# Kernel optimization log

Hardware: AMD Instinct MI355X
Metric: run time of the kernel (lower is better)

## Reference

```python
import jax, jax.numpy as jnp
import numpy as np

EMB = 1024
HEADS = 8
SEQ = 4096
LN_EPS = 1e-5


def _layernorm(x, g, b):
    mu = jnp.mean(x, axis=-1, keepdims=True)
    var = jnp.mean(jnp.square(x - mu), axis=-1, keepdims=True)
    return (x - mu) * jax.lax.rsqrt(var + LN_EPS) * g + b


def setup_inputs() -> dict:
    key = jax.random.key(0)
    ks = jax.random.split(key, 12)
    s = 1.0 / np.sqrt(EMB)
    sz = 1.0 / np.sqrt(EMB * HEADS)
    return {
        "history": jax.random.normal(ks[0], (SEQ, EMB), jnp.float32),
        "embdding": jax.random.normal(ks[1], (SEQ, EMB), jnp.float32),
        # per-head Linear weights, torch layout [out, in], stacked over heads
        "Wq_w": jax.random.uniform(ks[2], (HEADS, EMB, EMB), jnp.float32, -s, s),
        "Wq_b": jax.random.uniform(ks[3], (HEADS, EMB), jnp.float32, -s, s),
        "Wk_w": jax.random.uniform(ks[4], (HEADS, EMB, EMB), jnp.float32, -s, s),
        "Wk_b": jax.random.uniform(ks[5], (HEADS, EMB), jnp.float32, -s, s),
        "Wv_w": jax.random.uniform(ks[6], (HEADS, EMB, EMB), jnp.float32, -s, s),
        "Wv_b": jax.random.uniform(ks[7], (HEADS, EMB), jnp.float32, -s, s),
        "Wz_w": jax.random.uniform(ks[8], (EMB, EMB * HEADS), jnp.float32, -sz, sz),
        "Wz_b": jax.random.uniform(ks[9], (EMB,), jnp.float32, -sz, sz),
        "ln1_g": jnp.ones((EMB,), jnp.float32),
        "ln1_b": jnp.zeros((EMB,), jnp.float32),
        "Wf_w": jax.random.uniform(ks[10], (EMB, EMB), jnp.float32, -s, s),
        "Wf_b": jax.random.uniform(ks[11], (EMB,), jnp.float32, -s, s),
        "ln2_g": jnp.ones((EMB,), jnp.float32),
        "ln2_b": jnp.zeros((EMB,), jnp.float32),
    }


def reference(history, embdding, Wq_w, Wq_b, Wk_w, Wk_b, Wv_w, Wv_b,
              Wz_w, Wz_b, ln1_g, ln1_b, Wf_w, Wf_b, ln2_g, ln2_b):
    S, E = embdding.shape
    H = Wq_w.shape[0]
    # per-head linears (torch: y = x @ W.T + b), batched over heads
    Q = jnp.einsum('se,hfe->hsf', embdding, Wq_w) + Wq_b[:, None, :]  # [H,S,E]
    K = jnp.einsum('se,hfe->hsf', embdding, Wk_w) + Wk_b[:, None, :]
    V = jnp.einsum('se,hfe->hsf', history, Wv_w) + Wv_b[:, None, :]
    # K^T @ Q -> [H, E, E], softmax over dim=1 of the 2D matrix == last axis here
    scores = jnp.einsum('hse,hsf->hef', K, Q) / jnp.sqrt(jnp.asarray(E, Q.dtype))
    A = jax.nn.softmax(scores, axis=-1)  # [H,E,E]
    Zh = jnp.einsum('hse,hef->hsf', V, A)  # [H,S,E]
    Z = jnp.transpose(Zh, (1, 0, 2)).reshape(S, H * E)  # cat(dim=1) in head order
    O = Z @ Wz_w.T + Wz_b  # [S,E]
    LN1 = _layernorm(O, ln1_g, ln1_b) + embdding
    FN = LN1 @ Wf_w.T + Wf_b
    LN2 = _layernorm(FN, ln2_g, ln2_b) + LN1
    return LN2
```

## Files before the change

### kernel.cpp

```cpp
#include <hip/hip_runtime.h>


constexpr int EMB = 1024;
constexpr int SEQ = 4096;
constexpr int NH  = 8;

using f32x4  = __attribute__((ext_vector_type(4))) float;
using bf16x8 = __attribute__((ext_vector_type(8))) __bf16;
using us8    = __attribute__((ext_vector_type(8))) unsigned short;

#define GLOAD_LDS16(g, l) __builtin_amdgcn_global_load_lds(                 \
    (const __attribute__((address_space(1))) void*)(g),                     \
    (__attribute__((address_space(3))) void*)(l), 16, 0, 0)

__device__ inline unsigned short f2bf(float x) {
  unsigned int u = __float_as_uint(x);
  u += 0x7FFFu + ((u >> 16) & 1u);
  return (unsigned short)(u >> 16);
}
__device__ inline float bf2f(unsigned short h) {
  return __uint_as_float(((unsigned int)h) << 16);
}

constexpr int NB_DOTB = 4096;
constexpr int NB_ROWB = 1664;
constexpr int NB_XT   = 1024;

__global__ __launch_bounds__(256) void mega_cvt_k(
    const float* __restrict__ Wk, const float* __restrict__ Wq,
    const float* __restrict__ hist, const float* __restrict__ Wz,
    const float* __restrict__ Wf, const float* __restrict__ emb,
    const float* __restrict__ Wv, const float* __restrict__ xbar,
    unsigned short* __restrict__ Wkb, unsigned short* __restrict__ Wqb,
    unsigned short* __restrict__ Yb, unsigned short* __restrict__ Wzb,
    unsigned short* __restrict__ Wfb, unsigned short* __restrict__ XT,
    unsigned short* __restrict__ WvT,
    float* __restrict__ u, float* __restrict__ v) {
  __shared__ float tileT[64][65];
  const int b = blockIdx.x, tid = threadIdx.x;

  if (b < NB_DOTB) {
    int gw = b * 4 + (tid >> 6);
    int lane = tid & 63;
    const float* src = (gw < 8192) ? Wk : Wq;
    unsigned short* dst = (gw < 8192) ? Wkb : Wqb;
    float* dot = (gw < 8192) ? u : v;
    int row = gw & 8191;
    const float4* sr = (const float4*)(src + (size_t)row * EMB);
    const float4* xb4 = (const float4*)xbar;
    ushort4* d4 = (ushort4*)(dst + (size_t)row * EMB);
    float s = 0.f;
#pragma unroll
    for (int j = 0; j < 4; ++j) {
      int idx = j * 64 + lane;
      float4 x = sr[idx];
      float4 xb = xb4[idx];
      ushort4 o; o.x = f2bf(x.x); o.y = f2bf(x.y); o.z = f2bf(x.z); o.w = f2bf(x.w);
      d4[idx] = o;
      s += x.x * xb.x + x.y * xb.y + x.z * xb.z + x.w * xb.w;
    }
#pragma unroll
    for (int off = 32; off; off >>= 1) s += __shfl_down(s, off);
    if (lane == 0) dot[row] = s;
  } else if (b < NB_DOTB + NB_ROWB) {
    size_t f0 = (size_t)(b - NB_DOTB) * 8192;
    const float* src; unsigned short* dst; size_t loc;
    if (f0 < 4194304ull) { src = hist; dst = Yb; loc = f0; }
    else if (f0 < 12582912ull) { src = Wz; dst = Wzb; loc = f0 - 4194304ull; }
    else { src = Wf; dst = Wfb; loc = f0 - 12582912ull; }
#pragma unroll
    for (int p = 0; p < 8; ++p) {
      int i = p * 256 + tid;
      float4 x = ((const float4*)(src + loc))[i];
      ushort4 o; o.x = f2bf(x.x); o.y = f2bf(x.y); o.z = f2bf(x.z); o.w = f2bf(x.w);
      ((ushort4*)(dst + loc))[i] = o;
    }
  } else {
    int tb = b - (NB_DOTB + NB_ROWB);
    const float* src; unsigned short* dst; int R, r0, c0;
    if (tb < NB_XT) {
      src = emb; dst = XT; R = SEQ;
      r0 = (tb >> 4) * 64; c0 = (tb & 15) * 64;
    } else {
      int t2 = tb - NB_XT, z = t2 >> 8, tt = t2 & 255;
      src = Wv + (size_t)z * EMB * EMB; dst = WvT + (size_t)z * EMB * EMB;
      R = EMB;
      r0 = (tt >> 4) * 64; c0 = (tt & 15) * 64;
    }
    int tx = tid & 15, ty = tid >> 4;
#pragma unroll
    for (int p = 0; p < 4; ++p) {
      int ir = p * 16 + ty;
      float4 x = *(const float4*)(src + (size_t)(r0 + ir) * EMB + c0 + tx * 4);
      tileT[tx * 4 + 0][ir] = x.x; tileT[tx * 4 + 1][ir] = x.y;
      tileT[tx * 4 + 2][ir] = x.z; tileT[tx * 4 + 3][ir] = x.w;
    }
    __syncthreads();
#pragma unroll
    for (int p = 0; p < 4; ++p) {
      int orow = p * 16 + ty;
      ushort4 o;
      o.x = f2bf(tileT[orow][tx * 4 + 0]);
      o.y = f2bf(tileT[orow][tx * 4 + 1]);
      o.z = f2bf(tileT[orow][tx * 4 + 2]);
      o.w = f2bf(tileT[orow][tx * 4 + 3]);
      *(ushort4*)(dst + (size_t)(c0 + orow) * R + r0 + tx * 4) = o;
    }
  }
}

__global__ __launch_bounds__(256) void colsum_part_k(const float* __restrict__ X,
                                                     float* __restrict__ part) {
  int e = blockIdx.x * 256 + threadIdx.x;
  int y = blockIdx.y;
  float s = 0.f;
  for (int r = y * 128; r < y * 128 + 128; ++r) s += X[(size_t)r * EMB + e];
  part[y * EMB + e] = s;
}
__global__ __launch_bounds__(256) void colsum_red_k(const float* __restrict__ part,
                                                    float* __restrict__ xbar) {
  int e = blockIdx.x * 256 + threadIdx.x;
  float s = 0.f;
  for (int y = 0; y < 32; ++y) s += part[y * EMB + e];
  xbar[e] = s;
}

__global__ __launch_bounds__(256) void dvec_k(const unsigned short* __restrict__ Wzb,
                                              const float* __restrict__ bz,
                                              const float* __restrict__ c,
                                              float* __restrict__ d) {
  __shared__ float sb[4];
  int g = blockIdx.x, tid = threadIdx.x;
  const unsigned short* row = Wzb + (size_t)g * (NH * EMB);
  float s = 0.f;
#pragma unroll
  for (int p = 0; p < 4; ++p) {
    int i = p * 256 + tid;
    us8 w = ((const us8*)row)[i];
    float4 c0 = ((const float4*)c)[i * 2];
    float4 c1 = ((const float4*)c)[i * 2 + 1];
    s += bf2f(w[0]) * c0.x + bf2f(w[1]) * c0.y + bf2f(w[2]) * c0.z + bf2f(w[3]) * c0.w;
    s += bf2f(w[4]) * c1.x + bf2f(w[5]) * c1.y + bf2f(w[6]) * c1.z + bf2f(w[7]) * c1.w;
  }
  int lane = tid & 63, w = tid >> 6;
#pragma unroll
  for (int off = 32; off; off >>= 1) s += __shfl_down(s, off);
  if (lane == 0) sb[w] = s;
  __syncthreads();
  if (tid == 0) d[g] = bz[g] + sb[0] + sb[1] + sb[2] + sb[3];
}

__global__ __launch_bounds__(256) void mred_tr_k(const unsigned short* __restrict__ Mp,
                                                 unsigned short* __restrict__ MT) {
  __shared__ float t[32][33];
  int g0 = blockIdx.x * 32, e0 = blockIdx.y * 32;
  int tx = threadIdx.x & 31, ty = threadIdx.x >> 5;
#pragma unroll
  for (int k = 0; k < 4; ++k) {
    int e = e0 + ty + k * 8;
    float s = 0.f;
#pragma unroll
    for (int h = 0; h < NH; ++h)
      s += bf2f(Mp[((size_t)h << 20) + (size_t)e * EMB + g0 + tx]);
    t[ty + k * 8][tx] = s;
  }
  __syncthreads();
#pragma unroll
  for (int k = 0; k < 4; ++k) {
    int r = ty + k * 8;
    MT[(size_t)(g0 + r) * EMB + e0 + tx] = f2bf(t[tx][r]);
  }
}

__global__ __launch_bounds__(256) void gram_red_k(const unsigned short* __restrict__ Gp,
                                                  unsigned short* __restrict__ Gbf) {
  int i = blockIdx.x * 256 + threadIdx.x;
  float4 s = {0.f, 0.f, 0.f, 0.f};
#pragma unroll
  for (int z = 0; z < 8; ++z) {
    ushort4 v = ((const ushort4*)(Gp + (size_t)z * EMB * EMB))[i];
    s.x += bf2f(v.x); s.y += bf2f(v.y); s.z += bf2f(v.z); s.w += bf2f(v.w);
  }
  ushort4 o; o.x = f2bf(s.x); o.y = f2bf(s.y); o.z = f2bf(s.z); o.w = f2bf(s.w);
  ((ushort4*)Gbf)[i] = o;
}

__global__ __launch_bounds__(256) void colstat1_k(const unsigned short* __restrict__ ScT,
                                                  float* __restrict__ m_part,
                                                  float* __restrict__ s_part) {
  int col = blockIdx.x * 256 + threadIdx.x;
  int rc = blockIdx.y, h = blockIdx.z;
  const unsigned short* base = ScT + ((size_t)h * EMB + rc * 64) * EMB + col;
  float m = -1e30f, s = 0.f;
#pragma unroll 4
  for (int r = 0; r < 64; ++r) {
    float x = bf2f(base[(size_t)r * EMB]);
    float nm = fmaxf(m, x);
    s = s * __expf(m - nm) + __expf(x - nm);
    m = nm;
  }
  m_part[((size_t)h * 16 + rc) * EMB + col] = m;
  s_part[((size_t)h * 16 + rc) * EMB + col] = s;
}

__global__ __launch_bounds__(256) void colstat2_k(const float* __restrict__ m_part,
                                                  const float* __restrict__ s_part,
                                                  float* __restrict__ mfin,
                                                  float* __restrict__ isfin) {
  int i = blockIdx.x * 256 + threadIdx.x;
  int h = i >> 10, col = i & 1023;
  float M = -1e30f, S = 0.f;
#pragma unroll
  for (int c = 0; c < 16; ++c) {
    float m = m_part[((size_t)h * 16 + c) * EMB + col];
    float s = s_part[((size_t)h * 16 + c) * EMB + col];
    float nm = fmaxf(M, m);
    S = S * __expf(M - nm) + s * __expf(m - nm);
    M = nm;
  }
  mfin[i] = M;
  isfin[i] = 1.0f / S;
}

__global__ __launch_bounds__(256) void at_cvec_k(const unsigned short* __restrict__ ScT,
                                                 const float* __restrict__ mfin,
                                                 const float* __restrict__ isfin,
                                                 const float* __restrict__ bv,
                                                 unsigned short* __restrict__ AT,
                                                 float* __restrict__ cbuf) {
  __shared__ float sb[4];
  int f = blockIdx.x, h = blockIdx.y, tid = threadIdx.x;
  size_t rowoff = ((size_t)h * EMB + f) * EMB;
  ushort4 xr = ((const ushort4*)(ScT + rowoff))[tid];
  float4 m  = ((const float4*)(mfin + (size_t)h * EMB))[tid];
  float4 is = ((const float4*)(isfin + (size_t)h * EMB))[tid];
  float4 b  = ((const float4*)(bv + (size_t)h * EMB))[tid];
  float a0 = __expf(bf2f(xr.x) - m.x) * is.x;
  float a1 = __expf(bf2f(xr.y) - m.y) * is.y;
  float a2 = __expf(bf2f(xr.z) - m.z) * is.z;
  float a3 = __expf(bf2f(xr.w) - m.w) * is.w;
  ushort4 o; o.x = f2bf(a0); o.y = f2bf(a1); o.z = f2bf(a2); o.w = f2bf(a3);
  ((ushort4*)(AT + rowoff))[tid] = o;
  float s = a0 * b.x + a1 * b.y + a2 * b.z + a3 * b.w;
  int lane = tid & 63, w = tid >> 6;
#pragma unroll
  for (int off = 32; off; off >>= 1) s += __shfl_down(s, off);
  if (lane == 0) sb[w] = s;
  __syncthreads();
  if (tid == 0) cbuf[h * EMB + f] = sb[0] + sb[1] + sb[2] + sb[3];
}

__global__ __launch_bounds__(256) void layernorm_k(const float* __restrict__ Xin,
                                                   const float* __restrict__ resid,
                                                   const float* __restrict__ gw,
                                                   const float* __restrict__ bw,
                                                   float* __restrict__ outf,
                                                   unsigned short* __restrict__ outb) {
  __shared__ float sb[16];
  int row = blockIdx.x, tid = threadIdx.x;
  float4 v = ((const float4*)(Xin + (size_t)row * EMB))[tid];
  float s = v.x + v.y + v.z + v.w;
  float q = v.x * v.x + v.y * v.y + v.z * v.z + v.w * v.w;
  int lane = tid & 63, w = tid >> 6;
#pragma unroll
  for (int off = 32; off; off >>= 1) { s += __shfl_down(s, off); q += __shfl_down(q, off); }
  if (lane == 0) { sb[w] = s; sb[8 + w] = q; }
  __syncthreads();
  float mu  = (sb[0] + sb[1] + sb[2] + sb[3]) * (1.0f / EMB);
  float var = (sb[8] + sb[9] + sb[10] + sb[11]) * (1.0f / EMB) - mu * mu;
  float rs = rsqrtf(var + 1e-5f);
  float4 rv = ((const float4*)(resid + (size_t)row * EMB))[tid];
  float4 gv = ((const float4*)gw)[tid];
  float4 bv = ((const float4*)bw)[tid];
  float o0 = (v.x - mu) * rs * gv.x + bv.x + rv.x;
  float o1 = (v.y - mu) * rs * gv.y + bv.y + rv.y;
  float o2 = (v.z - mu) * rs * gv.z + bv.z + rv.z;
  float o3 = (v.w - mu) * rs * gv.w + bv.w + rv.w;
  float4 ov; ov.x = o0; ov.y = o1; ov.z = o2; ov.w = o3;
  ((float4*)(outf + (size_t)row * EMB))[tid] = ov;
  if (outb) {
    ushort4 ob; ob.x = f2bf(o0); ob.y = f2bf(o1); ob.z = f2bf(o2); ob.w = f2bf(o3);
    ((ushort4*)(outb + (size_t)row * EMB))[tid] = ob;
  }
}

template <int MODE>
__global__ __launch_bounds__(256) void gemm_nt(const unsigned short* __restrict__ A,
                                               const unsigned short* __restrict__ B,
                                               void* __restrict__ Cout,
                                               int K, int lda, int ldb, int ldc,
                                               long long aZ, long long bZ, long long cZ,
                                               int nx, int ny,
                                               const float* __restrict__ e0,
                                               const float* __restrict__ e1,
                                               const float* __restrict__ e2,
                                               const float* __restrict__ e3) {
  const int q = gridDim.x >> 3;
  const int wg = (blockIdx.x & 7) * q + (blockIdx.x >> 3);
  const int bx = wg % nx;
  const int by = (wg / nx) % ny;
  const int z  = wg / (nx * ny);
  A += (size_t)z * aZ;
  B += (size_t)z * bZ;
  const int tid = threadIdx.x;
  const int lane = tid & 63, wid = tid >> 6;
  const int wm = wid >> 1, wn = wid & 1;
  const int row0 = bx * 128, col0 = by * 128;

  __shared__ __align__(16) unsigned short As[2][128 * 64];
  __shared__ __align__(16) unsigned short Bs[2][128 * 64];

  f32x4 acc[4][4] = {};
  const int lrow = lane & 15, kg = lane >> 4;
  const int lr = lane >> 3;
  const int lc = (lane & 7) * 8;

  auto stage = [&](int buf, int k0) {
#pragma unroll
    for (int c = 0; c < 4; ++c) {
      int chunk = wid * 4 + c;
      int r = chunk * 8 + lr;
      GLOAD_LDS16(A + (size_t)(row0 + r) * lda + k0 + lc, &As[buf][chunk * 512]);
      GLOAD_LDS16(B + (size_t)(col0 + r) * ldb + k0 + lc, &Bs[buf][chunk * 512]);
    }
  };

  stage(0, 0);
  __syncthreads();

  const int nt = K >> 6;
  for (int t = 0; t < nt; ++t) {
    const int cur = t & 1;
    if (t + 1 < nt) stage(cur ^ 1, (t + 1) << 6);
#pragma unroll
    for (int ks = 0; ks < 2; ++ks) {
      bf16x8 a[4], b[4];
      int koff = ks * 32 + kg * 8;
#pragma unroll
      for (int i = 0; i < 4; ++i)
        a[i] = *(const bf16x8*)&As[cur][(wm * 64 + i * 16 + lrow) * 64 + koff];
#pragma unroll
      for (int j = 0; j < 4; ++j)
        b[j] = *(const bf16x8*)&Bs[cur][(wn * 64 + j * 16 + lrow) * 64 + koff];
#pragma unroll
      for (int i = 0; i < 4; ++i)
#pragma unroll
        for (int j = 0; j < 4; ++j)
          acc[i][j] = __builtin_amdgcn_mfma_f32_16x16x32_bf16(a[i], b[j], acc[i][j], 0, 0, 0);
    }
    __syncthreads();
  }

  const int rb = (lane >> 4) * 4, cc = lane & 15;
  if (MODE == 1 || MODE == 4) {
    unsigned short* Cs = &As[0][0];
#pragma unroll
    for (int i = 0; i < 4; ++i) {
#pragma unroll
      for (int j = 0; j < 4; ++j) {
#pragma unroll
        for (int r = 0; r < 4; ++r) {
          float val = acc[i][j][r];
          int mm = wm * 64 + i * 16 + rb + r;
          int nn = wn * 64 + j * 16 + cc;
          if (MODE == 4) {
            int m = row0 + mm, n = col0 + nn;
            float bq = e0[z * EMB + m], uu = e1[z * EMB + n];
            float bk = e2[z * EMB + n], vv = e3[z * EMB + m];
            val = (val + bq * (uu + (float)SEQ * bk) + vv * bk) * (1.0f / 32.0f);
          }
          Cs[mm * 128 + nn] = f2bf(val);
        }
      }
    }
    __syncthreads();
    unsigned short* Cg = (unsigned short*)Cout + (size_t)z * cZ;
#pragma unroll
    for (int p = 0; p < 8; ++p) {
      int idx = p * 256 + tid;
      int row = idx >> 4, col = (idx & 15) * 8;
      *(us8*)(Cg + (size_t)(row0 + row) * ldc + col0 + col) =
          *(const us8*)&Cs[row * 128 + col];
    }
  } else {
#pragma unroll
    for (int i = 0; i < 4; ++i) {
#pragma unroll
      for (int j = 0; j < 4; ++j) {
#pragma unroll
        for (int r = 0; r < 4; ++r) {
          int m = row0 + wm * 64 + i * 16 + rb + r;
          int n = col0 + wn * 64 + j * 16 + cc;
          size_t off = (size_t)z * cZ + (size_t)m * ldc + n;
          ((float*)Cout)[off] = acc[i][j][r] + e0[n];
        }
      }
    }
  }
}

extern "C" void kernel_launch(void* const* d_in, const int* in_sizes, int n_in,
                              void* d_out, int out_size, void* d_ws, size_t ws_size,
                              hipStream_t stream) {
  const float* history = (const float*)d_in[0];
  const float* emb     = (const float*)d_in[1];
  const float* Wq_w = (const float*)d_in[2];
  const float* Wq_b = (const float*)d_in[3];
  const float* Wk_w = (const float*)d_in[4];
  const float* Wk_b = (const float*)d_in[5];
  const float* Wv_w = (const float*)d_in[6];
  const float* Wv_b = (const float*)d_in[7];
  const float* Wz_w = (const float*)d_in[8];
  const float* Wz_b = (const float*)d_in[9];
  const float* ln1_g = (const float*)d_in[10];
  const float* ln1_b = (const float*)d_in[11];
  const float* Wf_w = (const float*)d_in[12];
  const float* Wf_b = (const float*)d_in[13];
  const float* ln2_g = (const float*)d_in[14];
  const float* ln2_b = (const float*)d_in[15];

  char* ws = (char*)d_ws;
  const size_t MB = 1024ull * 1024ull;
  unsigned short* XT  = (unsigned short*)(ws + 0);
  unsigned short* Ybf = (unsigned short*)(ws + 8 * MB);
  unsigned short* Wkb = (unsigned short*)(ws + 16 * MB);
  unsigned short* Wqb = (unsigned short*)(ws + 32 * MB);
  unsigned short* WvT = (unsigned short*)(ws + 48 * MB);
  unsigned short* Wzb = (unsigned short*)(ws + 64 * MB);
  unsigned short* Wfb = (unsigned short*)(ws + 80 * MB);
  unsigned short* Gbf = (unsigned short*)(ws + 82 * MB);
  float* xpart = (float*)(ws + 84 * MB);
  float* xbar  = (float*)(ws + 84 * MB + 160 * 1024);
  float* ubuf  = (float*)(ws + 84 * MB + 192 * 1024);
  float* vbuf  = (float*)(ws + 84 * MB + 256 * 1024);
  float* cbuf  = (float*)(ws + 84 * MB + 320 * 1024);
  float* dbuf  = (float*)(ws + 84 * MB + 384 * 1024);
  unsigned short* Tbf = (unsigned short*)(ws + 85 * MB);
  float* Sc  = (float*)(ws + 101 * MB);
  char*  St  = ws + 133 * MB;
  unsigned short* ATb = (unsigned short*)(ws + 149 * MB);
  unsigned short* MTb = (unsigned short*)(ws + 165 * MB);
  float* m_part = (float*)(St);
  float* s_part = (float*)(St + 512 * 1024);
  float* mfin   = (float*)(St + 1024 * 1024);
  float* isfin  = (float*)(St + 1056 * 1024);
  unsigned short* Gp  = (unsigned short*)Sc;
  unsigned short* ScT = (unsigned short*)Sc;
  unsigned short* Cbf = Tbf;
  unsigned short* Mp  = (unsigned short*)Sc;
  float* Obuf = (float*)St;
  float* LN1  = (float*)ATb;
  unsigned short* LN1b = XT;
  float* FN   = (float*)Tbf;

  colsum_part_k<<<dim3(4, 32), 256, 0, stream>>>(emb, xpart);
  colsum_red_k<<<dim3(4), 256, 0, stream>>>(xpart, xbar);

  mega_cvt_k<<<dim3(8832), 256, 0, stream>>>(Wk_w, Wq_w, history, Wz_w, Wf_w,
                                             emb, Wv_w, xbar,
                                             Wkb, Wqb, Ybf, Wzb, Wfb, XT, WvT,
                                             ubuf, vbuf);

  gemm_nt<1><<<dim3(512), 256, 0, stream>>>(XT, XT, Gp, 512, SEQ, SEQ, EMB,
                                            512, 512, (long long)EMB * EMB, 8, 8,
                                            nullptr, nullptr, nullptr, nullptr);
  gram_red_k<<<dim3(EMB * EMB / 4 / 256), 256, 0, stream>>>(Gp, Gbf);
  gemm_nt<1><<<dim3(512), 256, 0, stream>>>(Wqb, Gbf, Tbf, EMB, EMB, EMB, EMB,
                                            (long long)EMB * EMB, 0, (long long)EMB * EMB, 8, 8,
                                            nullptr, nullptr, nullptr, nullptr);
  gemm_nt<4><<<dim3(512), 256, 0, stream>>>(Tbf, Wkb, ScT, EMB, EMB, EMB, EMB,
                                            (long long)EMB * EMB, (long long)EMB * EMB,
                                            (long long)EMB * EMB, 8, 8,
                                            Wq_b, ubuf, Wk_b, vbuf);
  colstat1_k<<<dim3(4, 16, NH), 256, 0, stream>>>(ScT, m_part, s_part);
  colstat2_k<<<dim3(32), 256, 0, stream>>>(m_part, s_part, mfin, isfin);
  at_cvec_k<<<dim3(EMB, NH), 256, 0, stream>>>(ScT, mfin, isfin, Wv_b, ATb, cbuf);
  gemm_nt<1><<<dim3(512), 256, 0, stream>>>(WvT, ATb, Cbf, EMB, EMB, EMB, EMB,
                                            (long long)EMB * EMB, (long long)EMB * EMB,
                                            (long long)EMB * EMB, 8, 8,
                                            nullptr, nullptr, nullptr, nullptr);
  gemm_nt<1><<<dim3(512), 256, 0, stream>>>(Cbf, Wzb, Mp, EMB, EMB, NH * EMB, EMB,
                                            (long long)EMB * EMB, (long long)EMB,
                                            (long long)EMB * EMB, 8, 8,
                                            nullptr, nullptr, nullptr, nullptr);
  mred_tr_k<<<dim3(EMB / 32, EMB / 32), 256, 0, stream>>>(Mp, MTb);
  dvec_k<<<dim3(EMB), 256, 0, stream>>>(Wzb, Wz_b, cbuf, dbuf);
  gemm_nt<3><<<dim3(256), 256, 0, stream>>>(Ybf, MTb, Obuf, EMB, EMB, EMB, EMB,
                                            0, 0, 0, 32, 8,
                                            dbuf, nullptr, nullptr, nullptr);
  layernorm_k<<<dim3(SEQ), 256, 0, stream>>>(Obuf, emb, ln1_g, ln1_b, LN1, LN1b);
  gemm_nt<3><<<dim3(256), 256, 0, stream>>>(LN1b, Wfb, FN, EMB, EMB, EMB, EMB,
                                            0, 0, 0, 32, 8,
                                            Wf_b, nullptr, nullptr, nullptr);
  layernorm_k<<<dim3(SEQ), 256, 0, stream>>>(FN, LN1, ln2_g, ln2_b, (float*)d_out, nullptr);
}
```

Baseline: 298.2 us.

## Fuse fp32-to-bf16 conversion of weights and history into GEMM tile loads

Drops the standalone conversion pass that wrote bf16 copies of Wk, Wq, Wz, Wf and history. The GEMMs now take fp32 operands directly and convert them to bf16 while loading each tile into LDS, using register loads in place of the async global-to-LDS path. The row dot products and the dvec reduction now read the fp32 weights directly. This removes a large bf16 write and re-read, but costs in-kernel conversion, synchronous loads that lose the direct-to-LDS copy, and repeated reading of fp32 data (twice the bytes) across tiles.

```diff
diff --git a/kernel.cpp b/kernel.cpp
--- a/kernel.cpp
+++ b/kernel.cpp
@@ -22,91 +22,66 @@
   return __uint_as_float(((unsigned int)h) << 16);
 }
 
-constexpr int NB_DOTB = 4096;
-constexpr int NB_ROWB = 1664;
-constexpr int NB_XT   = 1024;
-
-__global__ __launch_bounds__(256) void mega_cvt_k(
-    const float* __restrict__ Wk, const float* __restrict__ Wq,
-    const float* __restrict__ hist, const float* __restrict__ Wz,
-    const float* __restrict__ Wf, const float* __restrict__ emb,
-    const float* __restrict__ Wv, const float* __restrict__ xbar,
-    unsigned short* __restrict__ Wkb, unsigned short* __restrict__ Wqb,
-    unsigned short* __restrict__ Yb, unsigned short* __restrict__ Wzb,
-    unsigned short* __restrict__ Wfb, unsigned short* __restrict__ XT,
-    unsigned short* __restrict__ WvT,
-    float* __restrict__ u, float* __restrict__ v) {
+__global__ __launch_bounds__(256) void cvt_tr_k(const float* __restrict__ emb,
+                                                const float* __restrict__ Wv,
+                                                unsigned short* __restrict__ XT,
+                                                unsigned short* __restrict__ WvT) {
   __shared__ float tileT[64][65];
   const int b = blockIdx.x, tid = threadIdx.x;
-
-  if (b < NB_DOTB) {
-    int gw = b * 4 + (tid >> 6);
-    int lane = tid & 63;
-    const float* src = (gw < 8192) ? Wk : Wq;
-    unsigned short* dst = (gw < 8192) ? Wkb : Wqb;
-    float* dot = (gw < 8192) ? u : v;
-    int row = gw & 8191;
-    const float4* sr = (const float4*)(src + (size_t)row * EMB);
-    const float4* xb4 = (const float4*)xbar;
-    ushort4* d4 = (ushort4*)(dst + (size_t)row * EMB);
-    float s = 0.f;
-#pragma unroll
-    for (int j = 0; j < 4; ++j) {
-      int idx = j * 64 + lane;
-      float4 x = sr[idx];
-      float4 xb = xb4[idx];
-      ushort4 o; o.x = f2bf(x.x); o.y = f2bf(x.y); o.z = f2bf(x.z); o.w = f2bf(x.w);
-      d4[idx] = o;
-      s += x.x * xb.x + x.y * xb.y + x.z * xb.z + x.w * xb.w;
-    }
-#pragma unroll
-    for (int off = 32; off; off >>= 1) s += __shfl_down(s, off);
-    if (lane == 0) dot[row] = s;
-  } else if (b < NB_DOTB + NB_ROWB) {
-    size_t f0 = (size_t)(b - NB_DOTB) * 8192;
-    const float* src; unsigned short* dst; size_t loc;
-    if (f0 < 4194304ull) { src = hist; dst = Yb; loc = f0; }
-    else if (f0 < 12582912ull) { src = Wz; dst = Wzb; loc = f0 - 4194304ull; }
-    else { src = Wf; dst = Wfb; loc = f0 - 12582912ull; }
-#pragma unroll
-    for (int p = 0; p < 8; ++p) {
-      int i = p * 256 + tid;
-      float4 x = ((const float4*)(src + loc))[i];
-      ushort4 o; o.x = f2bf(x.x); o.y = f2bf(x.y); o.z = f2bf(x.z); o.w = f2bf(x.w);
-      ((ushort4*)(dst + loc))[i] = o;
-    }
+  const float* src; unsigned short* dst; int R, r0, c0;
+  if (b < 1024) {
+    src = emb; dst = XT; R = SEQ;
+    r0 = (b >> 4) * 64; c0 = (b & 15) * 64;
   } else {
-    int tb = b - (NB_DOTB + NB_ROWB);
-    const float* src; unsigned short* dst; int R, r0, c0;
-    if (tb < NB_XT) {
-      src = emb; dst = XT; R = SEQ;
-      r0 = (tb >> 4) * 64; c0 = (tb & 15) * 64;
-    } else {
-      int t2 = tb - NB_XT, z = t2 >> 8, tt = t2 & 255;
-      src = Wv + (size_t)z * EMB * EMB; dst = WvT + (size_t)z * EMB * EMB;
-      R = EMB;
-      r0 = (tt >> 4) * 64; c0 = (tt & 15) * 64;
-    }
-    int tx = tid & 15, ty = tid >> 4;
-#pragma unroll
-    for (int p = 0; p < 4; ++p) {
-      int ir = p * 16 + ty;
-      float4 x = *(const float4*)(src + (size_t)(r0 + ir) * EMB + c0 + tx * 4);
-      tileT[tx * 4 + 0][ir] = x.x; tileT[tx * 4 + 1][ir] = x.y;
-      tileT[tx * 4 + 2][ir] = x.z; tileT[tx * 4 + 3][ir] = x.w;
-    }
-    __syncthreads();
-#pragma unroll
-    for (int p = 0; p < 4; ++p) {
-      int orow = p * 16 + ty;
-      ushort4 o;
-      o.x = f2bf(tileT[orow][tx * 4 + 0]);
-      o.y = f2bf(tileT[orow][tx * 4 + 1]);
-      o.z = f2bf(tileT[orow][tx * 4 + 2]);
-      o.w = f2bf(tileT[orow][tx * 4 + 3]);
-      *(ushort4*)(dst + (size_t)(c0 + orow) * R + r0 + tx * 4) = o;
-    }
-  }
+    int t2 = b - 1024, z = t2 >> 8, tt = t2 & 255;
+    src = Wv + (size_t)z * EMB * EMB; dst = WvT + (size_t)z * EMB * EMB;
+    R = EMB;
+    r0 = (tt >> 4) * 64; c0 = (tt & 15) * 64;
+  }
+  int tx = tid & 15, ty = tid >> 4;
+#pragma unroll
+  for (int p = 0; p < 4; ++p) {
+    int ir = p * 16 + ty;
+    float4 x = *(const float4*)(src + (size_t)(r0 + ir) * EMB + c0 + tx * 4);
+    tileT[tx * 4 + 0][ir] = x.x; tileT[tx * 4 + 1][ir] = x.y;
+    tileT[tx * 4 + 2][ir] = x.z; tileT[tx * 4 + 3][ir] = x.w;
+  }
+  __syncthreads();
+#pragma unroll
+  for (int p = 0; p < 4; ++p) {
+    int orow = p * 16 + ty;
+    ushort4 o;
+    o.x = f2bf(tileT[orow][tx * 4 + 0]);
+    o.y = f2bf(tileT[orow][tx * 4 + 1]);
+    o.z = f2bf(tileT[orow][tx * 4 + 2]);
+    o.w = f2bf(tileT[orow][tx * 4 + 3]);
+    *(ushort4*)(dst + (size_t)(c0 + orow) * R + r0 + tx * 4) = o;
+  }
+}
+
+__global__ __launch_bounds__(256) void uv_k(const float* __restrict__ Wk,
+                                            const float* __restrict__ Wq,
+                                            const float* __restrict__ xbar,
+                                            float* __restrict__ u,
+                                            float* __restrict__ v) {
+  int gw = blockIdx.x * 4 + (threadIdx.x >> 6);
+  int lane = threadIdx.x & 63;
+  const float* src = (gw < 8192) ? Wk : Wq;
+  float* dot = (gw < 8192) ? u : v;
+  int row = gw & 8191;
+  const float4* sr  = (const float4*)(src + (size_t)row * EMB);
+  const float4* xb4 = (const float4*)xbar;
+  float s = 0.f;
+#pragma unroll
+  for (int j = 0; j < 4; ++j) {
+    int idx = j * 64 + lane;
+    float4 x = sr[idx];
+    float4 xb = xb4[idx];
+    s += x.x * xb.x + x.y * xb.y + x.z * xb.z + x.w * xb.w;
+  }
+#pragma unroll
+  for (int off = 32; off; off >>= 1) s += __shfl_down(s, off);
+  if (lane == 0) dot[row] = s;
 }
 
 __global__ __launch_bounds__(256) void colsum_part_k(const float* __restrict__ X,
@@ -125,22 +100,20 @@
   xbar[e] = s;
 }
 
-__global__ __launch_bounds__(256) void dvec_k(const unsigned short* __restrict__ Wzb,
+__global__ __launch_bounds__(256) void dvec_k(const float* __restrict__ Wz,
                                               const float* __restrict__ bz,
                                               const float* __restrict__ c,
                                               float* __restrict__ d) {
   __shared__ float sb[4];
   int g = blockIdx.x, tid = threadIdx.x;
-  const unsigned short* row = Wzb + (size_t)g * (NH * EMB);
+  const float* row = Wz + (size_t)g * (NH * EMB);
   float s = 0.f;
 #pragma unroll
-  for (int p = 0; p < 4; ++p) {
+  for (int p = 0; p < 8; ++p) {
     int i = p * 256 + tid;
-    us8 w = ((const us8*)row)[i];
-    float4 c0 = ((const float4*)c)[i * 2];
-    float4 c1 = ((const float4*)c)[i * 2 + 1];
-    s += bf2f(w[0]) * c0.x + bf2f(w[1]) * c0.y + bf2f(w[2]) * c0.z + bf2f(w[3]) * c0.w;
-    s += bf2f(w[4]) * c1.x + bf2f(w[5]) * c1.y + bf2f(w[6]) * c1.z + bf2f(w[7]) * c1.w;
+    float4 w = ((const float4*)row)[i];
+    float4 cv = ((const float4*)c)[i];
+    s += w.x * cv.x + w.y * cv.y + w.z * cv.z + w.w * cv.w;
   }
   int lane = tid & 63, w = tid >> 6;
 #pragma unroll
@@ -284,9 +257,9 @@
   }
 }
 
-template <int MODE>
-__global__ __launch_bounds__(256) void gemm_nt(const unsigned short* __restrict__ A,
-                                               const unsigned short* __restrict__ B,
+template <int MODE, int AF32, int BF32>
+__global__ __launch_bounds__(256) void gemm_nt(const void* __restrict__ Av,
+                                               const void* __restrict__ Bv,
                                                void* __restrict__ Cout,
                                                int K, int lda, int ldb, int ldc,
                                                long long aZ, long long bZ, long long cZ,
@@ -300,8 +273,10 @@
   const int bx = wg % nx;
   const int by = (wg / nx) % ny;
   const int z  = wg / (nx * ny);
-  A += (size_t)z * aZ;
-  B += (size_t)z * bZ;
+  const unsigned short* A16 = AF32 ? nullptr : (const unsigned short*)Av + (size_t)z * aZ;
+  const unsigned short* B16 = BF32 ? nullptr : (const unsigned short*)Bv + (size_t)z * bZ;
+  const float* A32 = AF32 ? (const float*)Av + (size_t)z * aZ : nullptr;
+  const float* B32 = BF32 ? (const float*)Bv + (size_t)z * bZ : nullptr;
   const int tid = threadIdx.x;
   const int lane = tid & 63, wid = tid >> 6;
   const int wm = wid >> 1, wn = wid & 1;
@@ -320,8 +295,28 @@
     for (int c = 0; c < 4; ++c) {
       int chunk = wid * 4 + c;
       int r = chunk * 8 + lr;
-      GLOAD_LDS16(A + (size_t)(row0 + r) * lda + k0 + lc, &As[buf][chunk * 512]);
-      GLOAD_LDS16(B + (size_t)(col0 + r) * ldb + k0 + lc, &Bs[buf][chunk * 512]);
+      if (AF32) {
+        const float* src = A32 + (size_t)(row0 + r) * lda + k0 + lc;
+        float4 x0 = *(const float4*)src;
+        float4 x1 = *(const float4*)(src + 4);
+        us8 o;
+        o[0] = f2bf(x0.x); o[1] = f2bf(x0.y); o[2] = f2bf(x0.z); o[3] = f2bf(x0.w);
+        o[4] = f2bf(x1.x); o[5] = f2bf(x1.y); o[6] = f2bf(x1.z); o[7] = f2bf(x1.w);
+        *(us8*)&As[buf][chunk * 512 + lane * 8] = o;
+      } else {
+        GLOAD_LDS16(A16 + (size_t)(row0 + r) * lda + k0 + lc, &As[buf][chunk * 512]);
+      }
+      if (BF32) {
+        const float* src = B32 + (size_t)(col0 + r) * ldb + k0 + lc;
+        float4 x0 = *(const float4*)src;
+        float4 x1 = *(const float4*)(src + 4);
+        us8 o;
+        o[0] = f2bf(x0.x); o[1] = f2bf(x0.y); o[2] = f2bf(x0.z); o[3] = f2bf(x0.w);
+        o[4] = f2bf(x1.x); o[5] = f2bf(x1.y); o[6] = f2bf(x1.z); o[7] = f2bf(x1.w);
+        *(us8*)&Bs[buf][chunk * 512 + lane * 8] = o;
+      } else {
+        GLOAD_LDS16(B16 + (size_t)(col0 + r) * ldb + k0 + lc, &Bs[buf][chunk * 512]);
+      }
     }
   };
 
@@ -422,12 +417,7 @@
   char* ws = (char*)d_ws;
   const size_t MB = 1024ull * 1024ull;
   unsigned short* XT  = (unsigned short*)(ws + 0);
-  unsigned short* Ybf = (unsigned short*)(ws + 8 * MB);
-  unsigned short* Wkb = (unsigned short*)(ws + 16 * MB);
-  unsigned short* Wqb = (unsigned short*)(ws + 32 * MB);
   unsigned short* WvT = (unsigned short*)(ws + 48 * MB);
-  unsigned short* Wzb = (unsigned short*)(ws + 64 * MB);
-  unsigned short* Wfb = (unsigned short*)(ws + 80 * MB);
   unsigned short* Gbf = (unsigned short*)(ws + 82 * MB);
   float* xpart = (float*)(ws + 84 * MB);
   float* xbar  = (float*)(ws + 84 * MB + 160 * 1024);
@@ -452,45 +442,41 @@
   float* LN1  = (float*)ATb;
   unsigned short* LN1b = XT;
   float* FN   = (float*)Tbf;
+  const long long EE = (long long)EMB * EMB;
 
   colsum_part_k<<<dim3(4, 32), 256, 0, stream>>>(emb, xpart);
   colsum_red_k<<<dim3(4), 256, 0, stream>>>(xpart, xbar);
-
-  mega_cvt_k<<<dim3(8832), 256, 0, stream>>>(Wk_w, Wq_w, history, Wz_w, Wf_w,
-                                             emb, Wv_w, xbar,
-                                             Wkb, Wqb, Ybf, Wzb, Wfb, XT, WvT,
-                                             ubuf, vbuf);
-
-  gemm_nt<1><<<dim3(512), 256, 0, stream>>>(XT, XT, Gp, 512, SEQ, SEQ, EMB,
-                                            512, 512, (long long)EMB * EMB, 8, 8,
-                                            nullptr, nullptr, nullptr, nullptr);
+  uv_k<<<dim3(4096), 256, 0, stream>>>(Wk_w, Wq_w, xbar, ubuf, vbuf);
+
+  cvt_tr_k<<<dim3(3072), 256, 0, stream>>>(emb, Wv_w, XT, WvT);
+
+  gemm_nt<1, 0, 0><<<dim3(512), 256, 0, stream>>>(XT, XT, Gp, 512, SEQ, SEQ, EMB,
+                                                  512, 512, EE, 8, 8,
+                                                  nullptr, nullptr, nullptr, nullptr);
   gram_red_k<<<dim3(EMB * EMB / 4 / 256), 256, 0, stream>>>(Gp, Gbf);
-  gemm_nt<1><<<dim3(512), 256, 0, stream>>>(Wqb, Gbf, Tbf, EMB, EMB, EMB, EMB,
-                                            (long long)EMB * EMB, 0, (long long)EMB * EMB, 8, 8,
-                                            nullptr, nullptr, nullptr, nullptr);
-  gemm_nt<4><<<dim3(512), 256, 0, stream>>>(Tbf, Wkb, ScT, EMB, EMB, EMB, EMB,
-                                            (long long)EMB * EMB, (long long)EMB * EMB,
-                                            (long long)EMB * EMB, 8, 8,
-                                            Wq_b, ubuf, Wk_b, vbuf);
+  gemm_nt<1, 1, 0><<<dim3(512), 256, 0, stream>>>(Wq_w, Gbf, Tbf, EMB, EMB, EMB, EMB,
+                                                  EE, 0, EE, 8, 8,
+                                                  nullptr, nullptr, nullptr, nullptr);
+  gemm_nt<4, 0, 1><<<dim3(512), 256, 0, stream>>>(Tbf, Wk_w, ScT, EMB, EMB, EMB, EMB,
+                                                  EE, EE, EE, 8, 8,
+                                                  Wq_b, ubuf, Wk_b, vbuf);
   colstat1_k<<<dim3(4, 16, NH), 256, 0, stream>>>(ScT, m_part, s_part);
   colstat2_k<<<dim3(32), 256, 0, stream>>>(m_part, s_part, mfin, isfin);
   at_cvec_k<<<dim3(EMB, NH), 256, 0, stream>>>(ScT, mfin, isfin, Wv_b, ATb, cbuf);
-  gemm_nt<1><<<dim3(512), 256, 0, stream>>>(WvT, ATb, Cbf, EMB, EMB, EMB, EMB,
-                                            (long long)EMB * EMB, (long long)EMB * EMB,
-                                            (long long)EMB * EMB, 8, 8,
-                                            nullptr, nullptr, nullptr, nullptr);
-  gemm_nt<1><<<dim3(512), 256, 0, stream>>>(Cbf, Wzb, Mp, EMB, EMB, NH * EMB, EMB,
-                                            (long long)EMB * EMB, (long long)EMB,
-                                            (long long)EMB * EMB, 8, 8,
-                                            nullptr, nullptr, nullptr, nullptr);
+  gemm_nt<1, 0, 0><<<dim3(512), 256, 0, stream>>>(WvT, ATb, Cbf, EMB, EMB, EMB, EMB,
+                                                  EE, EE, EE, 8, 8,
+                                                  nullptr, nullptr, nullptr, nullptr);
+  gemm_nt<1, 0, 1><<<dim3(512), 256, 0, stream>>>(Cbf, Wz_w, Mp, EMB, EMB, NH * EMB, EMB,
+                                                  EE, (long long)EMB, EE, 8, 8,
+                                                  nullptr, nullptr, nullptr, nullptr);
   mred_tr_k<<<dim3(EMB / 32, EMB / 32), 256, 0, stream>>>(Mp, MTb);
-  dvec_k<<<dim3(EMB), 256, 0, stream>>>(Wzb, Wz_b, cbuf, dbuf);
-  gemm_nt<3><<<dim3(256), 256, 0, stream>>>(Ybf, MTb, Obuf, EMB, EMB, EMB, EMB,
-                                            0, 0, 0, 32, 8,
-                                            dbuf, nullptr, nullptr, nullptr);
+  dvec_k<<<dim3(EMB), 256, 0, stream>>>(Wz_w, Wz_b, cbuf, dbuf);
+  gemm_nt<3, 1, 0><<<dim3(256), 256, 0, stream>>>(history, MTb, Obuf, EMB, EMB, EMB, EMB,
+                                                  0, 0, 0, 32, 8,
+                                                  dbuf, nullptr, nullptr, nullptr);
   layernorm_k<<<dim3(SEQ), 256, 0, stream>>>(Obuf, emb, ln1_g, ln1_b, LN1, LN1b);
-  gemm_nt<3><<<dim3(256), 256, 0, stream>>>(LN1b, Wfb, FN, EMB, EMB, EMB, EMB,
-                                            0, 0, 0, 32, 8,
-                                            Wf_b, nullptr, nullptr, nullptr);
+  gemm_nt<3, 0, 1><<<dim3(256), 256, 0, stream>>>(LN1b, Wf_w, FN, EMB, EMB, EMB, EMB,
+                                                  0, 0, 0, 32, 8,
+                                                  Wf_b, nullptr, nullptr, nullptr);
   layernorm_k<<<dim3(SEQ), 256, 0, stream>>>(FN, LN1, ln2_g, ln2_b, (float*)d_out, nullptr);
 }
```

New measurement: 318.7 us. 6.9% more time.

## Halve GEMM M-tile to 64 and drop LDS double buffering for occupancy

Applied to the files above, without the earlier changes.

The shared NT GEMM kernel moves from a 128x128 tile to a 64x128 tile. Each wave now holds 2x4 accumulators, and the double-buffered LDS staging becomes a single buffer with a sync after each load, cutting LDS from 64KB to 24KB per block. All launches double their grid sizes to match, so there are more workgroups to fill the CUs and higher occupancy. In exchange, global loads no longer overlap compute within a block, operand reuse per tile drops, and there are more blocks to schedule.

```diff
diff --git a/kernel.cpp b/kernel.cpp
--- a/kernel.cpp
+++ b/kernel.cpp
@@ -305,45 +305,45 @@
   const int tid = threadIdx.x;
   const int lane = tid & 63, wid = tid >> 6;
   const int wm = wid >> 1, wn = wid & 1;
-  const int row0 = bx * 128, col0 = by * 128;
-
-  __shared__ __align__(16) unsigned short As[2][128 * 64];
-  __shared__ __align__(16) unsigned short Bs[2][128 * 64];
-
-  f32x4 acc[4][4] = {};
+  const int row0 = bx * 64, col0 = by * 128;
+
+  __shared__ __align__(16) unsigned short lds[(64 + 128) * 64];
+  unsigned short* As = lds;
+  unsigned short* Bs = lds + 64 * 64;
+
+  f32x4 acc[2][4] = {};
   const int lrow = lane & 15, kg = lane >> 4;
   const int lr = lane >> 3;
   const int lc = (lane & 7) * 8;
 
-  auto stage = [&](int buf, int k0) {
+  const int nt = K >> 6;
+  for (int t = 0; t < nt; ++t) {
+    const int k0 = t << 6;
+#pragma unroll
+    for (int c = 0; c < 2; ++c) {
+      int chunk = wid * 2 + c;
+      int r = chunk * 8 + lr;
+      GLOAD_LDS16(A + (size_t)(row0 + r) * lda + k0 + lc, &As[chunk * 512]);
+    }
 #pragma unroll
     for (int c = 0; c < 4; ++c) {
       int chunk = wid * 4 + c;
       int r = chunk * 8 + lr;
-      GLOAD_LDS16(A + (size_t)(row0 + r) * lda + k0 + lc, &As[buf][chunk * 512]);
-      GLOAD_LDS16(B + (size_t)(col0 + r) * ldb + k0 + lc, &Bs[buf][chunk * 512]);
-    }
-  };
-
-  stage(0, 0);
-  __syncthreads();
-
-  const int nt = K >> 6;
-  for (int t = 0; t < nt; ++t) {
-    const int cur = t & 1;
-    if (t + 1 < nt) stage(cur ^ 1, (t + 1) << 6);
+      GLOAD_LDS16(B + (size_t)(col0 + r) * ldb + k0 + lc, &Bs[chunk * 512]);
+    }
+    __syncthreads();
 #pragma unroll
     for (int ks = 0; ks < 2; ++ks) {
-      bf16x8 a[4], b[4];
+      bf16x8 a[2], b[4];
       int koff = ks * 32 + kg * 8;
 #pragma unroll
-      for (int i = 0; i < 4; ++i)
-        a[i] = *(const bf16x8*)&As[cur][(wm * 64 + i * 16 + lrow) * 64 + koff];
+      for (int i = 0; i < 2; ++i)
+        a[i] = *(const bf16x8*)&As[(wm * 32 + i * 16 + lrow) * 64 + koff];
 #pragma unroll
       for (int j = 0; j < 4; ++j)
-        b[j] = *(const bf16x8*)&Bs[cur][(wn * 64 + j * 16 + lrow) * 64 + koff];
-#pragma unroll
-      for (int i = 0; i < 4; ++i)
+        b[j] = *(const bf16x8*)&Bs[(wn * 64 + j * 16 + lrow) * 64 + koff];
+#pragma unroll
+      for (int i = 0; i < 2; ++i)
 #pragma unroll
         for (int j = 0; j < 4; ++j)
           acc[i][j] = __builtin_amdgcn_mfma_f32_16x16x32_bf16(a[i], b[j], acc[i][j], 0, 0, 0);
@@ -353,15 +353,15 @@
 
   const int rb = (lane >> 4) * 4, cc = lane & 15;
   if (MODE == 1 || MODE == 4) {
-    unsigned short* Cs = &As[0][0];
-#pragma unroll
-    for (int i = 0; i < 4; ++i) {
+    unsigned short* Cs = lds;
+#pragma unroll
+    for (int i = 0; i < 2; ++i) {
 #pragma unroll
       for (int j = 0; j < 4; ++j) {
 #pragma unroll
         for (int r = 0; r < 4; ++r) {
           float val = acc[i][j][r];
-          int mm = wm * 64 + i * 16 + rb + r;
+          int mm = wm * 32 + i * 16 + rb + r;
           int nn = wn * 64 + j * 16 + cc;
           if (MODE == 4) {
             int m = row0 + mm, n = col0 + nn;
@@ -376,7 +376,7 @@
     __syncthreads();
     unsigned short* Cg = (unsigned short*)Cout + (size_t)z * cZ;
 #pragma unroll
-    for (int p = 0; p < 8; ++p) {
+    for (int p = 0; p < 4; ++p) {
       int idx = p * 256 + tid;
       int row = idx >> 4, col = (idx & 15) * 8;
       *(us8*)(Cg + (size_t)(row0 + row) * ldc + col0 + col) =
@@ -384,12 +384,12 @@
     }
   } else {
 #pragma unroll
-    for (int i = 0; i < 4; ++i) {
+    for (int i = 0; i < 2; ++i) {
 #pragma unroll
       for (int j = 0; j < 4; ++j) {
 #pragma unroll
         for (int r = 0; r < 4; ++r) {
-          int m = row0 + wm * 64 + i * 16 + rb + r;
+          int m = row0 + wm * 32 + i * 16 + rb + r;
           int n = col0 + wn * 64 + j * 16 + cc;
           size_t off = (size_t)z * cZ + (size_t)m * ldc + n;
           ((float*)Cout)[off] = acc[i][j][r] + e0[n];
@@ -452,6 +452,7 @@
   float* LN1  = (float*)ATb;
   unsigned short* LN1b = XT;
   float* FN   = (float*)Tbf;
+  const long long EE = (long long)EMB * EMB;
 
   colsum_part_k<<<dim3(4, 32), 256, 0, stream>>>(emb, xpart);
   colsum_red_k<<<dim3(4), 256, 0, stream>>>(xpart, xbar);
@@ -461,36 +462,33 @@
                                              Wkb, Wqb, Ybf, Wzb, Wfb, XT, WvT,
                                              ubuf, vbuf);
 
-  gemm_nt<1><<<dim3(512), 256, 0, stream>>>(XT, XT, Gp, 512, SEQ, SEQ, EMB,
-                                            512, 512, (long long)EMB * EMB, 8, 8,
-                                            nullptr, nullptr, nullptr, nullptr);
+  gemm_nt<1><<<dim3(1024), 256, 0, stream>>>(XT, XT, Gp, 512, SEQ, SEQ, EMB,
+                                             512, 512, EE, 16, 8,
+                                             nullptr, nullptr, nullptr, nullptr);
   gram_red_k<<<dim3(EMB * EMB / 4 / 256), 256, 0, stream>>>(Gp, Gbf);
-  gemm_nt<1><<<dim3(512), 256, 0, stream>>>(Wqb, Gbf, Tbf, EMB, EMB, EMB, EMB,
-                                            (long long)EMB * EMB, 0, (long long)EMB * EMB, 8, 8,
-                                            nullptr, nullptr, nullptr, nullptr);
-  gemm_nt<4><<<dim3(512), 256, 0, stream>>>(Tbf, Wkb, ScT, EMB, EMB, EMB, EMB,
-                                            (long long)EMB * EMB, (long long)EMB * EMB,
-                                            (long long)EMB * EMB, 8, 8,
-                                            Wq_b, ubuf, Wk_b, vbuf);
+  gemm_nt<1><<<dim3(1024), 256, 0, stream>>>(Wqb, Gbf, Tbf, EMB, EMB, EMB, EMB,
+                                             EE, 0, EE, 16, 8,
+                                             nullptr, nullptr, nullptr, nullptr);
+  gemm_nt<4><<<dim3(1024), 256, 0, stream>>>(Tbf, Wkb, ScT, EMB, EMB, EMB, EMB,
+                                             EE, EE, EE, 16, 8,
+                                             Wq_b, ubuf, Wk_b, vbuf);
   colstat1_k<<<dim3(4, 16, NH), 256, 0, stream>>>(ScT, m_part, s_part);
   colstat2_k<<<dim3(32), 256, 0, stream>>>(m_part, s_part, mfin, isfin);
   at_cvec_k<<<dim3(EMB, NH), 256, 0, stream>>>(ScT, mfin, isfin, Wv_b, ATb, cbuf);
-  gemm_nt<1><<<dim3(512), 256, 0, stream>>>(WvT, ATb, Cbf, EMB, EMB, EMB, EMB,
-                                            (long long)EMB * EMB, (long long)EMB * EMB,
-                                            (long long)EMB * EMB, 8, 8,
-                                            nullptr, nullptr, nullptr, nullptr);
-  gemm_nt<1><<<dim3(512), 256, 0, stream>>>(Cbf, Wzb, Mp, EMB, EMB, NH * EMB, EMB,
-                                            (long long)EMB * EMB, (long long)EMB,
-                                            (long long)EMB * EMB, 8, 8,
-                                            nullptr, nullptr, nullptr, nullptr);
+  gemm_nt<1><<<dim3(1024), 256, 0, stream>>>(WvT, ATb, Cbf, EMB, EMB, EMB, EMB,
+                                             EE, EE, EE, 16, 8,
+                                             nullptr, nullptr, nullptr, nullptr);
+  gemm_nt<1><<<dim3(1024), 256, 0, stream>>>(Cbf, Wzb, Mp, EMB, EMB, NH * EMB, EMB,
+                                             EE, (long long)EMB, EE, 16, 8,
+                                             nullptr, nullptr, nullptr, nullptr);
   mred_tr_k<<<dim3(EMB / 32, EMB / 32), 256, 0, stream>>>(Mp, MTb);
   dvec_k<<<dim3(EMB), 256, 0, stream>>>(Wzb, Wz_b, cbuf, dbuf);
-  gemm_nt<3><<<dim3(256), 256, 0, stream>>>(Ybf, MTb, Obuf, EMB, EMB, EMB, EMB,
-                                            0, 0, 0, 32, 8,
+  gemm_nt<3><<<dim3(512), 256, 0, stream>>>(Ybf, MTb, Obuf, EMB, EMB, EMB, EMB,
+                                            0, 0, 0, 64, 8,
                                             dbuf, nullptr, nullptr, nullptr);
   layernorm_k<<<dim3(SEQ), 256, 0, stream>>>(Obuf, emb, ln1_g, ln1_b, LN1, LN1b);
-  gemm_nt<3><<<dim3(256), 256, 0, stream>>>(LN1b, Wfb, FN, EMB, EMB, EMB, EMB,
-                                            0, 0, 0, 32, 8,
+  gemm_nt<3><<<dim3(512), 256, 0, stream>>>(LN1b, Wfb, FN, EMB, EMB, EMB, EMB,
+                                            0, 0, 0, 64, 8,
                                             Wf_b, nullptr, nullptr, nullptr);
   layernorm_k<<<dim3(SEQ), 256, 0, stream>>>(FN, LN1, ln2_g, ln2_b, (float*)d_out, nullptr);
 }
```

Result: no change. 292.6 us (-1.9%).
